# Performance work log

Hardware: AMD Instinct MI355X
Metric: run time of the kernel (lower is better)

The kernel has to match this reference:

```python
import jax, jax.numpy as jnp
import numpy as np

B, S, IN, H = 8, 8192, 64, 256
HEADS, DH, M, L = 8, 32, 64, 4
FF, NC = 4 * H, 2


def setup_inputs() -> dict:
    key = jax.random.key(0)
    ks = jax.random.split(key, 16)
    w = lambda k, shape, s=0.02: jax.random.normal(k, shape, jnp.float32) * s
    return {
        "x": jax.random.normal(ks[0], (B, S, IN), jnp.float32),
        "emb_w": w(ks[1], (IN, H)), "emb_b": jnp.zeros((H,), jnp.float32),
        "pos": jax.random.normal(ks[2], (1, S, H), jnp.float32),
        "ln1_g": jnp.ones((L, H), jnp.float32), "ln1_b": jnp.zeros((L, H), jnp.float32),
        "wq": w(ks[3], (L, H, H)), "wk": w(ks[4], (L, H, H)), "wv": w(ks[5], (L, H, H)),
        "wo": w(ks[6], (L, H, H)), "bo": jnp.zeros((L, H), jnp.float32),
        "ln2_g": jnp.ones((L, H), jnp.float32), "ln2_b": jnp.zeros((L, H), jnp.float32),
        "w1": w(ks[7], (L, H, FF)), "b1": jnp.zeros((L, FF), jnp.float32),
        "w2": w(ks[8], (L, FF, H)), "b2": jnp.zeros((L, H), jnp.float32),
        "proj": jax.random.normal(ks[9], (L, M, DH), jnp.float32),  # FAVOR+ random features (buffer)
        "fc_w": w(ks[10], (H, NC)), "fc_b": jnp.zeros((NC,), jnp.float32),
    }


def layer_norm(x, g, b, eps=1e-5):
    mu = jnp.mean(x, -1, keepdims=True)
    var = jnp.mean(jnp.square(x - mu), -1, keepdims=True)
    return (x - mu) * jax.lax.rsqrt(var + eps) * g + b


def softmax_kernel(x, proj, is_query, eps=1e-4):
    # performer_pytorch FAVOR+ softmax kernel. x: [b,h,n,d], proj: [m,d]
    normalizer = x.shape[-1] ** -0.25
    ratio = proj.shape[0] ** -0.5
    xp = jnp.einsum('bhnd,md->bhnm', x * normalizer, proj)
    diag = jnp.sum(jnp.square(x), -1, keepdims=True) * (0.5 * normalizer * normalizer)
    if is_query:
        mx = jnp.max(xp, axis=-1, keepdims=True)
    else:
        mx = jnp.max(xp, axis=(-1, -2), keepdims=True)
    return ratio * (jnp.exp(xp - diag - mx) + eps)


def performer_attn(x, wq, wk, wv, wo, bo, proj):
    b, s, h = x.shape
    split = lambda t: t.reshape(b, s, HEADS, DH).transpose(0, 2, 1, 3)
    q, k, v = split(x @ wq), split(x @ wk), split(x @ wv)
    qp = softmax_kernel(q, proj, True)   # [b,h,n,m]
    kp = softmax_kernel(k, proj, False)  # [b,h,n,m]
    d_inv = 1.0 / jnp.einsum('bhnm,bhm->bhn', qp, jnp.sum(kp, axis=2))
    context = jnp.einsum('bhnm,bhne->bhme', kp, v)       # [b,h,m,dh]
    out = jnp.einsum('bhnm,bhme->bhne', qp, context) * d_inv[..., None]
    out = out.transpose(0, 2, 1, 3).reshape(b, s, h)
    return out @ wo + bo


def reference(x, emb_w, emb_b, pos, ln1_g, ln1_b, wq, wk, wv, wo, bo,
              ln2_g, ln2_b, w1, b1, w2, b2, proj, fc_w, fc_b):
    h = x @ emb_w + emb_b + pos[:, :x.shape[1], :]
    for l in range(L):
        h = h + performer_attn(layer_norm(h, ln1_g[l], ln1_b[l]),
                               wq[l], wk[l], wv[l], wo[l], bo[l], proj[l])
        hn = layer_norm(h, ln2_g[l], ln2_b[l])
        h = h + (jax.nn.gelu(hn @ w1[l] + b1[l], approximate=False) @ w2[l] + b2[l])
    pooled = jnp.mean(h, axis=1)
    return pooled @ fc_w + fc_b
```

## Files before the change

kernel.cpp:

```cpp
#include <hip/hip_runtime.h>
#include <math.h>

typedef unsigned short u16;
typedef __attribute__((ext_vector_type(8))) short bf16x8;
typedef __attribute__((ext_vector_type(4))) float f32x4;

static constexpr int D_S = 8192;
static constexpr int D_L = 4;
static constexpr int TOK = 65536;
static constexpr float NORMALIZER = 0.4204482076268573f;
static constexpr float RATIO = 0.125f;
static constexpr float KEPS = 1e-4f;

static constexpr size_t OFF_H     = 0;
static constexpr size_t OFF_XNB   = 16777216;
static constexpr size_t OFF_BIG   = 25165824;
static constexpr size_t OFF_V     = 41943040;
static constexpr size_t OFF_WKP   = 46137344;
static constexpr size_t OFF_WQP   = 46268416;
static constexpr size_t OFF_WK    = 46399488;
static constexpr size_t OFF_WQ    = 46465024;
static constexpr size_t OFF_WV    = 46530560;
static constexpr size_t OFF_WO    = 46596096;
static constexpr size_t OFF_W1    = 46661632;
static constexpr size_t OFF_W2    = 46923776;
static constexpr size_t OFF_DG    = 47185920;
static constexpr size_t OFF_KMAX  = 47710208;
static constexpr size_t OFF_PART  = 47710272;
static constexpr size_t OFF_PARTK = 49807424;
static constexpr size_t OFF_CTX   = 49872960;
static constexpr size_t OFF_KSUM  = 50004032;
static constexpr size_t OFF_POOL  = 50008128;
static constexpr size_t NEED_BYTES = 200040704;

static constexpr int BTS = 136;

static __device__ __forceinline__ float bf2f(u16 u) {
  return __uint_as_float(((unsigned int)u) << 16);
}
static __device__ __forceinline__ u16 f2bf(float f) {
  unsigned int u = __float_as_uint(f);
  u = (u + 0x7fffu + ((u >> 16) & 1u)) >> 16;
  return (u16)u;
}
static __device__ __forceinline__ float geluf(float v) {
  return 0.5f * v * (1.f + erff(v * 0.70710678118654752f));
}
static __device__ __forceinline__ float dec_max(unsigned int mk) {
  return __uint_as_float((mk & 0x80000000u) ? (mk & 0x7fffffffu) : ~mk);
}

__global__ void report_kernel(float* out, float v) {
  if (threadIdx.x < 16) out[threadIdx.x] = v;
}

__global__ __launch_bounds__(256) void zero_kernel(float* p, int n) {
  int i = blockIdx.x * 256 + threadIdx.x;
  if (i < n) p[i] = 0.f;
}

__global__ __launch_bounds__(256) void xcvt_kernel(const float* __restrict__ x,
                                                   u16* __restrict__ xb) {
  int i4 = (blockIdx.x * 256 + threadIdx.x) * 4;
  float4 v = *(const float4*)(x + i4);
  u16 o[4] = {f2bf(v.x), f2bf(v.y), f2bf(v.z), f2bf(v.w)};
  *(uint2*)(xb + i4) = *(uint2*)o;
}

__global__ __launch_bounds__(256) void ln_kernel(
    const float* __restrict__ src, u16* __restrict__ dst,
    const float* __restrict__ g, const float* __restrict__ b) {
  int wv = threadIdx.x >> 6, lane = threadIdx.x & 63;
  int t = blockIdx.x * 4 + wv;
  const float4 v = *(const float4*)(src + (size_t)t * 256 + lane * 4);
  float s1 = v.x + v.y + v.z + v.w;
  float s2 = v.x * v.x + v.y * v.y + v.z * v.z + v.w * v.w;
  for (int off = 32; off; off >>= 1) {
    s1 += __shfl_xor(s1, off);
    s2 += __shfl_xor(s2, off);
  }
  float mu = s1 * (1.f / 256.f);
  float var = s2 * (1.f / 256.f) - mu * mu;
  float rs = rsqrtf(var + 1e-5f);
  float4 gg = *(const float4*)(g + lane * 4);
  float4 bb = *(const float4*)(b + lane * 4);
  u16 o0 = f2bf((v.x - mu) * rs * gg.x + bb.x);
  u16 o1 = f2bf((v.y - mu) * rs * gg.y + bb.y);
  u16 o2 = f2bf((v.z - mu) * rs * gg.z + bb.z);
  u16 o3 = f2bf((v.w - mu) * rs * gg.w + bb.w);
  uint2 pk;
  pk.x = (unsigned)o0 | ((unsigned)o1 << 16);
  pk.y = (unsigned)o2 | ((unsigned)o3 << 16);
  *(uint2*)(dst + (size_t)t * 256 + lane * 4) = pk;
}

__global__ __launch_bounds__(256) void wsplit_kernel(
    const float* __restrict__ W, u16* __restrict__ Wt, int K, int N, int nb) {
  int i = blockIdx.x * 256 + threadIdx.x;
  int k = i >> nb, n = i & (N - 1);
  float val = W[i];
  u16 hi = f2bf(val);
  u16 lo = f2bf(val - bf2f(hi));
  Wt[(size_t)n * 2 * K + k] = hi;
  Wt[(size_t)n * 2 * K + K + k] = lo;
}

__global__ __launch_bounds__(256) void wprep_kernel(
    const float* __restrict__ wk, const float* __restrict__ wq,
    const float* __restrict__ wv, const float* __restrict__ wo,
    const float* __restrict__ w1, const float* __restrict__ w2,
    const float* __restrict__ proj,
    u16* __restrict__ WKP, u16* __restrict__ WQP,
    u16* __restrict__ WKt, u16* __restrict__ WQt,
    u16* __restrict__ WVt, u16* __restrict__ WOt,
    u16* __restrict__ W1t, u16* __restrict__ W2t,
    unsigned int* __restrict__ kmaxk) {
  int gi = blockIdx.x * 256 + threadIdx.x;
  if (gi < 64) kmaxk[gi] = 0u;
  if (gi < 262144) {
    int i = gi & 131071;
    const float* w = (gi < 131072) ? wk : wq;
    u16* Wt = (gi < 131072) ? WKP : WQP;
    int k = i & 255, n = i >> 8;
    int head = n >> 6, m = n & 63;
    float s = 0.f;
#pragma unroll
    for (int d = 0; d < 32; ++d) s += w[k * 256 + head * 32 + d] * proj[m * 32 + d];
    Wt[(size_t)n * 256 + k] = f2bf(s * NORMALIZER);
  } else if (gi < 393216) {
    int i = gi - 262144;
    const float* W = (i < 65536) ? wk : wq;
    u16* T = (i < 65536) ? WKt : WQt;
    int j = i & 65535;
    int k = j >> 8, n = j & 255;
    T[(size_t)n * 256 + k] = f2bf(W[j]);
  } else if (gi < 524288) {
    int i = gi - 393216;
    const float* W = (i < 65536) ? wv : wo;
    u16* T = (i < 65536) ? WVt : WOt;
    int j = i & 65535;
    int k = j >> 8, n = j & 255;
    float val = W[j];
    u16 hi = f2bf(val);
    u16 lo = f2bf(val - bf2f(hi));
    T[(size_t)n * 512 + k] = hi;
    T[(size_t)n * 512 + 256 + k] = lo;
  } else if (gi < 786432) {
    int i = gi - 524288;
    int k = i >> 10, n = i & 1023;
    W1t[(size_t)n * 256 + k] = f2bf(w1[i]);
  } else {
    int i = gi - 786432;
    int k = i >> 8, n = i & 255;
    W2t[(size_t)n * 1024 + k] = f2bf(w2[i]);
  }
}

template <int EPI, int ACT, int ACC, int OBF, int KM>
__global__ __launch_bounds__(256) void mfma_gemm(
    const u16* __restrict__ A, const u16* __restrict__ Wt,
    const u16* __restrict__ Wt2,
    const float* __restrict__ bias, const float* __restrict__ posP,
    const u16* __restrict__ diagIn,
    float* __restrict__ outF, u16* __restrict__ outB,
    u16* __restrict__ diagOut, unsigned int* __restrict__ kmaxOut,
    int N, int K) {
  __shared__ __align__(16) u16 Als[4096];
  __shared__ __align__(16) u16 Bls[4096];
  const int K2 = K * KM;
  int tid = threadIdx.x;
  int yb = blockIdx.y;
  int bm = blockIdx.x * 128;
  const u16* Wp = Wt;
  int bn = yb * 128;
  if (EPI == 6 && yb >= 4) { Wp = Wt2; bn = (yb - 4) * 128; }
  int w = tid >> 6, lane = tid & 63;
  int wm = w >> 1, wn = w & 1;
  int lr = lane & 15, lq = lane >> 4;
  f32x4 acc[4][4];
#pragma unroll
  for (int i = 0; i < 4; ++i)
#pragma unroll
    for (int j = 0; j < 4; ++j) acc[i][j] = (f32x4){0.f, 0.f, 0.f, 0.f};
  int r0 = tid >> 2, q0 = tid & 3;
  for (int k0 = 0; k0 < K2; k0 += 32) {
    int kk = k0 + q0 * 8;
    int gka = kk & (K - 1);
    uint4 a0 = *(const uint4*)(A + (size_t)(bm + r0) * K + gka);
    uint4 a1 = *(const uint4*)(A + (size_t)(bm + r0 + 64) * K + gka);
    uint4 b0 = *(const uint4*)(Wp + (size_t)(bn + r0) * K2 + kk);
    uint4 b1 = *(const uint4*)(Wp + (size_t)(bn + r0 + 64) * K2 + kk);
    __syncthreads();
    ((uint4*)Als)[q0 * 128 + r0] = a0;
    ((uint4*)Als)[q0 * 128 + r0 + 64] = a1;
    ((uint4*)Bls)[q0 * 128 + r0] = b0;
    ((uint4*)Bls)[q0 * 128 + r0 + 64] = b1;
    __syncthreads();
    bf16x8 af[4], bfr[4];
#pragma unroll
    for (int mi = 0; mi < 4; ++mi)
      af[mi] = ((const bf16x8*)Als)[lq * 128 + wm * 64 + mi * 16 + lr];
#pragma unroll
    for (int ni = 0; ni < 4; ++ni)
      bfr[ni] = ((const bf16x8*)Bls)[lq * 128 + wn * 64 + ni * 16 + lr];
#pragma unroll
    for (int mi = 0; mi < 4; ++mi)
#pragma unroll
      for (int ni = 0; ni < 4; ++ni)
        acc[mi][ni] = __builtin_amdgcn_mfma_f32_16x16x32_bf16(af[mi], bfr[ni], acc[mi][ni], 0, 0, 0);
  }
  if (EPI == 0) {
#pragma unroll
    for (int ni = 0; ni < 4; ++ni) {
      int col = bn + wn * 64 + ni * 16 + lr;
      float bv = bias ? bias[col] : 0.f;
#pragma unroll
      for (int mi = 0; mi < 4; ++mi)
#pragma unroll
        for (int r = 0; r < 4; ++r) {
          int rowg = bm + wm * 64 + mi * 16 + lq * 4 + r;
          float val = acc[mi][ni][r] + bv;
          if (ACT) val = geluf(val);
          size_t o = (size_t)rowg * N + col;
          if (OBF) outB[o] = f2bf(val);
          else if (ACC) outF[o] += val;
          else outF[o] = val;
        }
    }
  }
  if (EPI == 3) {
    int head = (bn + wn * 64) >> 6;
#pragma unroll
    for (int mi = 0; mi < 4; ++mi) {
      float rm[4] = {-3.4e38f, -3.4e38f, -3.4e38f, -3.4e38f};
#pragma unroll
      for (int ni = 0; ni < 4; ++ni)
#pragma unroll
        for (int r = 0; r < 4; ++r) rm[r] = fmaxf(rm[r], acc[mi][ni][r]);
#pragma unroll
      for (int r = 0; r < 4; ++r) {
        float t = rm[r];
        t = fmaxf(t, __shfl_xor(t, 1)); t = fmaxf(t, __shfl_xor(t, 2));
        t = fmaxf(t, __shfl_xor(t, 4)); t = fmaxf(t, __shfl_xor(t, 8));
        rm[r] = t;
      }
#pragma unroll
      for (int r = 0; r < 4; ++r) {
        int rowg = bm + wm * 64 + mi * 16 + lq * 4 + r;
        float dg = bf2f(diagIn[(size_t)rowg * 16 + 8 + head]);
#pragma unroll
        for (int ni = 0; ni < 4; ++ni) {
          int col = bn + wn * 64 + ni * 16 + lr;
          float v = RATIO * (__expf(acc[mi][ni][r] - dg - rm[r]) + KEPS);
          outB[(size_t)rowg * N + col] = f2bf(v);
        }
      }
    }
  }
  if (EPI == 4) {
#pragma unroll
    for (int ni = 0; ni < 4; ++ni) {
      int col = bn + wn * 64 + ni * 16 + lr;
      float bv = bias[col];
#pragma unroll
      for (int mi = 0; mi < 4; ++mi)
#pragma unroll
        for (int r = 0; r < 4; ++r) {
          int rowg = bm + wm * 64 + mi * 16 + lq * 4 + r;
          outF[(size_t)rowg * 256 + col] =
              acc[mi][ni][r] + bv + posP[(size_t)(rowg & (D_S - 1)) * 256 + col];
        }
    }
  }
  if (EPI == 6) {
    if (yb < 4) {
      float mx = -3.4e38f;
#pragma unroll
      for (int mi = 0; mi < 4; ++mi)
#pragma unroll
        for (int ni = 0; ni < 4; ++ni)
#pragma unroll
          for (int r = 0; r < 4; ++r) {
            float v = acc[mi][ni][r];
            mx = fmaxf(mx, v);
            int rowg = bm + wm * 64 + mi * 16 + lq * 4 + r;
            int col = bn + wn * 64 + ni * 16 + lr;
            outB[(size_t)rowg * N + col] = f2bf(v);
          }
#pragma unroll
      for (int off = 1; off < 64; off <<= 1) mx = fmaxf(mx, __shfl_xor(mx, off));
      if (lane == 0) {
        int b = bm >> 13;
        int head = (bn + wn * 64) >> 6;
        unsigned int u = __float_as_uint(mx);
        unsigned int key = (u & 0x80000000u) ? ~u : (u | 0x80000000u);
        atomicMax(kmaxOut + b * 8 + head, key);
      }
    } else {
      const float c05n2 = 0.5f * NORMALIZER * NORMALIZER;
      int hb = (bn + wn * 64) >> 5;
#pragma unroll
      for (int mi = 0; mi < 4; ++mi) {
        float s0[4] = {0.f, 0.f, 0.f, 0.f}, s1[4] = {0.f, 0.f, 0.f, 0.f};
#pragma unroll
        for (int ni = 0; ni < 4; ++ni)
#pragma unroll
          for (int r = 0; r < 4; ++r) {
            float v = acc[mi][ni][r];
            if (ni < 2) s0[r] += v * v; else s1[r] += v * v;
          }
#pragma unroll
        for (int r = 0; r < 4; ++r) {
          float a = s0[r], b = s1[r];
          a += __shfl_xor(a, 1); a += __shfl_xor(a, 2); a += __shfl_xor(a, 4); a += __shfl_xor(a, 8);
          b += __shfl_xor(b, 1); b += __shfl_xor(b, 2); b += __shfl_xor(b, 4); b += __shfl_xor(b, 8);
          if (lr == 0) {
            int rowg = bm + wm * 64 + mi * 16 + lq * 4 + r;
            diagOut[(size_t)rowg * 16 + hb] = f2bf(c05n2 * a);
            diagOut[(size_t)rowg * 16 + hb + 1] = f2bf(c05n2 * b);
          }
        }
      }
    }
  }
}

__global__ __launch_bounds__(256) void ctxaccum_kernel(
    const u16* __restrict__ xp, const u16* __restrict__ v,
    const u16* __restrict__ dg, const unsigned int* __restrict__ kmaxk,
    float* __restrict__ part, float* __restrict__ partk, int hf) {
  __shared__ float kpS[64 * 64];
  __shared__ float vS[64 * 32];
  int tid = threadIdx.x;
  int bl = blockIdx.x >> 3, head = blockIdx.x & 7, c = blockIdx.y;
  int n0l = bl * 8192 + c * 512;
  int bhg = (hf * 4 + bl) * 8 + head;
  int tg0 = hf * 32768 + n0l;
  float mx = dec_max(kmaxk[bhg]);
  int m = tid & 63, eg = tid >> 6;
  float acc[8] = {};
  float ks = 0.f;
  const u16* kpb = xp + (size_t)tg0 * 512 + head * 64;
  const u16* vb = v + (size_t)n0l * 256 + head * 32;
  for (int tile = 0; tile < 8; ++tile) {
    int nb = tile * 64;
    __syncthreads();
#pragma unroll
    for (int i = 0; i < 2; ++i) {
      int idx8 = tid + i * 256;
      int row = idx8 >> 3, c8 = (idx8 & 7) * 8;
      float dgrow = bf2f(dg[(size_t)(tg0 + nb + row) * 16 + head]);
      u16 tmp[8];
      *(uint4*)tmp = *(const uint4*)(kpb + (size_t)(nb + row) * 512 + c8);
#pragma unroll
      for (int j = 0; j < 8; ++j)
        kpS[row * 64 + c8 + j] = RATIO * (__expf(bf2f(tmp[j]) - dgrow - mx) + KEPS);
    }
    {
      int row = tid >> 2, c8 = (tid & 3) * 8;
      u16 tmp[8];
      *(uint4*)tmp = *(const uint4*)(vb + (size_t)(nb + row) * 256 + c8);
#pragma unroll
      for (int j = 0; j < 8; ++j) vS[row * 32 + c8 + j] = bf2f(tmp[j]);
    }
    __syncthreads();
#pragma unroll 4
    for (int n = 0; n < 64; ++n) {
      float kv = kpS[n * 64 + m];
      if (eg == 0) ks += kv;
      const float* vr = &vS[n * 32 + eg * 8];
#pragma unroll
      for (int j = 0; j < 8; ++j) acc[j] += kv * vr[j];
    }
  }
  float* pp = part + ((size_t)bhg * 16 + c) * 2048 + m * 32 + eg * 8;
#pragma unroll
  for (int j = 0; j < 8; ++j) pp[j] = acc[j];
  if (eg == 0) partk[((size_t)bhg * 16 + c) * 64 + m] = ks;
}

__global__ __launch_bounds__(256) void ctxreduce_kernel(
    const float* __restrict__ part, const float* __restrict__ partk,
    float* __restrict__ ctx, float* __restrict__ ksum) {
  int bh = blockIdx.x, tid = threadIdx.x;
#pragma unroll
  for (int i = 0; i < 8; ++i) {
    int idx = tid + i * 256;
    float s = 0.f;
#pragma unroll
    for (int cc = 0; cc < 16; ++cc)
      s += part[((size_t)bh * 16 + cc) * 2048 + idx];
    ctx[(size_t)bh * 2048 + idx] = s;
  }
  if (tid < 64) {
    float s = 0.f;
#pragma unroll
    for (int cc = 0; cc < 16; ++cc) s += partk[((size_t)bh * 16 + cc) * 64 + tid];
    ksum[bh * 64 + tid] = s;
  }
}

__global__ __launch_bounds__(256) void btprep_kernel(
    const float* __restrict__ ctx, const float* __restrict__ ksum,
    u16* __restrict__ Bt) {
  int bh = blockIdx.x, tid = threadIdx.x;
  for (int idx = tid; idx < 48 * 64; idx += 256) {
    int n = idx >> 6, k = idx & 63;
    float v = 0.f;
    if (n < 32) v = ctx[(size_t)bh * 2048 + k * 32 + n];
    else if (n == 32) v = ksum[bh * 64 + k];
    u16 hi = f2bf(v);
    u16 lo = f2bf(v - bf2f(hi));
    u16* row = Bt + ((size_t)bh * 48 + n) * BTS;
    row[k] = hi;
    row[64 + k] = lo;
  }
}

__global__ __launch_bounds__(256) void attnout_kernel(
    const u16* __restrict__ qp, const u16* __restrict__ Bt,
    u16* __restrict__ ao, int hf) {
  __shared__ __align__(16) u16 BtS[48 * BTS];
  int tid = threadIdx.x;
  int rb = blockIdx.x, head = blockIdx.y;
  int t0l = rb * 128;
  int bhg = ((hf * 32768 + t0l) >> 13) * 8 + head;
  {
    const uint4* src = (const uint4*)(Bt + (size_t)bhg * 48 * BTS);
    for (int i = tid; i < 48 * BTS / 8; i += 256) ((uint4*)BtS)[i] = src[i];
  }
  __syncthreads();
  int w = tid >> 6, lane = tid & 63;
  int lr = lane & 15, lq = lane >> 4;
  int tw = t0l + w * 32;
  const u16* qpb = qp + (size_t)(hf * 32768 + tw) * 512 + head * 64;
  bf16x8 af[2][2];
#pragma unroll
  for (int mt = 0; mt < 2; ++mt)
#pragma unroll
    for (int kc = 0; kc < 2; ++kc)
      af[mt][kc] = *(const bf16x8*)(qpb + (size_t)(mt * 16 + lr) * 512 + kc * 32 + lq * 8);
  f32x4 c0[2], c1[2], c2[2];
#pragma unroll
  for (int mt = 0; mt < 2; ++mt) {
    c0[mt] = (f32x4){0.f, 0.f, 0.f, 0.f};
    c1[mt] = (f32x4){0.f, 0.f, 0.f, 0.f};
    c2[mt] = (f32x4){0.f, 0.f, 0.f, 0.f};
  }
#pragma unroll
  for (int kc = 0; kc < 4; ++kc) {
    bf16x8 b0 = *(const bf16x8*)(BtS + (size_t)(0 * 16 + lr) * BTS + kc * 32 + lq * 8);
    bf16x8 b1 = *(const bf16x8*)(BtS + (size_t)(1 * 16 + lr) * BTS + kc * 32 + lq * 8);
    bf16x8 b2 = *(const bf16x8*)(BtS + (size_t)(2 * 16 + lr) * BTS + kc * 32 + lq * 8);
#pragma unroll
    for (int mt = 0; mt < 2; ++mt) {
      bf16x8 a = af[mt][kc & 1];
      c0[mt] = __builtin_amdgcn_mfma_f32_16x16x32_bf16(a, b0, c0[mt], 0, 0, 0);
      c1[mt] = __builtin_amdgcn_mfma_f32_16x16x32_bf16(a, b1, c1[mt], 0, 0, 0);
      c2[mt] = __builtin_amdgcn_mfma_f32_16x16x32_bf16(a, b2, c2[mt], 0, 0, 0);
    }
  }
#pragma unroll
  for (int mt = 0; mt < 2; ++mt)
#pragma unroll
    for (int r = 0; r < 4; ++r) {
      float den = __shfl(c2[mt][r], lane & 48);
      int rowl = tw + mt * 16 + lq * 4 + r;
      float inv = 1.f / den;
      ao[(size_t)rowl * 256 + head * 32 + lr] = f2bf(c0[mt][r] * inv);
      ao[(size_t)rowl * 256 + head * 32 + 16 + lr] = f2bf(c1[mt][r] * inv);
    }
}

__global__ __launch_bounds__(256) void pool_kernel(
    const float* __restrict__ h, float* __restrict__ pooled) {
  int b = blockIdx.x, chunk = blockIdx.y, j = threadIdx.x;
  const float* hp = h + (size_t)(b * D_S + chunk * 256) * 256 + j;
  float acc = 0.f;
#pragma unroll 4
  for (int s = 0; s < 256; ++s) acc += hp[(size_t)s * 256];
  atomicAdd(pooled + b * 256 + j, acc);
}

__global__ __launch_bounds__(64) void final_kernel(
    const float* __restrict__ pooled, const float* __restrict__ fcw,
    const float* __restrict__ fcb, float* __restrict__ out) {
  int tid = threadIdx.x;
  if (tid >= 16) return;
  int b = tid >> 1, c = tid & 1;
  float acc = 0.f;
  for (int j = 0; j < 256; ++j) acc += pooled[b * 256 + j] * fcw[j * 2 + c];
  out[b * 2 + c] = acc * (1.f / 8192.f) + fcb[c];
}

extern "C" void kernel_launch(void* const* d_in, const int* in_sizes, int n_in,
                              void* d_out, int out_size, void* d_ws, size_t ws_size,
                              hipStream_t stream) {
  const float* x     = (const float*)d_in[0];
  const float* emb_w = (const float*)d_in[1];
  const float* emb_b = (const float*)d_in[2];
  const float* pos   = (const float*)d_in[3];
  const float* ln1_g = (const float*)d_in[4];
  const float* ln1_b = (const float*)d_in[5];
  const float* wq    = (const float*)d_in[6];
  const float* wk    = (const float*)d_in[7];
  const float* wv    = (const float*)d_in[8];
  const float* wo    = (const float*)d_in[9];
  const float* bo    = (const float*)d_in[10];
  const float* ln2_g = (const float*)d_in[11];
  const float* ln2_b = (const float*)d_in[12];
  const float* w1    = (const float*)d_in[13];
  const float* b1    = (const float*)d_in[14];
  const float* w2    = (const float*)d_in[15];
  const float* b2    = (const float*)d_in[16];
  const float* proj  = (const float*)d_in[17];
  const float* fc_w  = (const float*)d_in[18];
  const float* fc_b  = (const float*)d_in[19];

  if (ws_size < NEED_BYTES) {
    report_kernel<<<1, 64, 0, stream>>>((float*)d_out, (float)ws_size);
    return;
  }

  float* ws = (float*)d_ws;
  float* h      = ws + OFF_H;
  u16* xnb      = (u16*)(ws + OFF_XNB);
  u16* BIG      = (u16*)(ws + OFF_BIG);
  u16* Vb       = (u16*)(ws + OFF_V);
  u16* WKPt     = (u16*)(ws + OFF_WKP);
  u16* WQPt     = (u16*)(ws + OFF_WQP);
  u16* WKt      = (u16*)(ws + OFF_WK);
  u16* WQt      = (u16*)(ws + OFF_WQ);
  u16* WVt      = (u16*)(ws + OFF_WV);
  u16* WOt      = (u16*)(ws + OFF_WO);
  u16* W1t      = (u16*)(ws + OFF_W1);
  u16* W2t      = (u16*)(ws + OFF_W2);
  u16* dg       = (u16*)(ws + OFF_DG);
  unsigned int* kmaxk = (unsigned int*)(ws + OFF_KMAX);
  float* part   = ws + OFF_PART;
  u16* Bt       = (u16*)(ws + OFF_PART);
  float* partk  = ws + OFF_PARTK;
  float* ctx    = ws + OFF_CTX;
  float* ksum   = ws + OFF_KSUM;
  float* pooled = ws + OFF_POOL;

  xcvt_kernel<<<4096, 256, 0, stream>>>(x, BIG);
  wsplit_kernel<<<64, 256, 0, stream>>>(emb_w, WKPt, 64, 256, 8);
  mfma_gemm<4, 0, 0, 0, 2><<<dim3(512, 2), 256, 0, stream>>>(
      BIG, WKPt, nullptr, emb_b, pos, nullptr, h, nullptr, nullptr, nullptr, 256, 64);

  for (int l = 0; l < D_L; ++l) {
    const float* pj = proj + l * 2048;
    ln_kernel<<<TOK / 4, 256, 0, stream>>>(h, xnb, ln1_g + l * 256, ln1_b + l * 256);
    wprep_kernel<<<4096, 256, 0, stream>>>(
        wk + l * 65536, wq + l * 65536, wv + l * 65536, wo + l * 65536,
        w1 + l * 262144, w2 + l * 262144, pj,
        WKPt, WQPt, WKt, WQt, WVt, WOt, W1t, W2t, kmaxk);

    mfma_gemm<6, 0, 0, 1, 1><<<dim3(512, 8), 256, 0, stream>>>(
        xnb, WKPt, WKt, nullptr, nullptr, nullptr, nullptr, BIG, dg, kmaxk, 512, 256);
    for (int hf = 0; hf < 2; ++hf) {
      const u16* xh = xnb + (size_t)hf * 32768 * 256;
      mfma_gemm<0, 0, 0, 1, 2><<<dim3(256, 2), 256, 0, stream>>>(
          xh, WVt, nullptr, nullptr, nullptr, nullptr, nullptr, Vb, nullptr, nullptr, 256, 256);
      ctxaccum_kernel<<<dim3(32, 16), 256, 0, stream>>>(BIG, Vb, dg, kmaxk, part, partk, hf);
    }
    ctxreduce_kernel<<<64, 256, 0, stream>>>(part, partk, ctx, ksum);
    btprep_kernel<<<64, 256, 0, stream>>>(ctx, ksum, Bt);
    mfma_gemm<3, 0, 0, 1, 1><<<dim3(512, 4), 256, 0, stream>>>(
        xnb, WQPt, nullptr, nullptr, nullptr, dg, nullptr, BIG, nullptr, nullptr, 512, 256);
    for (int hf = 0; hf < 2; ++hf) {
      float* hh = h + (size_t)hf * 32768 * 256;
      attnout_kernel<<<dim3(256, 8), 256, 0, stream>>>(BIG, Bt, Vb, hf);
      mfma_gemm<0, 0, 1, 0, 2><<<dim3(256, 2), 256, 0, stream>>>(
          Vb, WOt, nullptr, bo + l * 256, nullptr, nullptr, hh, nullptr, nullptr, nullptr, 256, 256);
    }

    ln_kernel<<<TOK / 4, 256, 0, stream>>>(h, xnb, ln2_g + l * 256, ln2_b + l * 256);
    for (int hf = 0; hf < 2; ++hf) {
      const u16* xh = xnb + (size_t)hf * 32768 * 256;
      float* hh = h + (size_t)hf * 32768 * 256;
      mfma_gemm<0, 1, 0, 1, 1><<<dim3(256, 8), 256, 0, stream>>>(
          xh, W1t, nullptr, b1 + l * 1024, nullptr, nullptr, nullptr, BIG, nullptr, nullptr, 1024, 256);
      mfma_gemm<0, 0, 1, 0, 1><<<dim3(256, 2), 256, 0, stream>>>(
          BIG, W2t, nullptr, b2 + l * 256, nullptr, nullptr, hh, nullptr, nullptr, nullptr, 256, 1024);
    }
  }

  zero_kernel<<<8, 256, 0, stream>>>(pooled, 2048);
  pool_kernel<<<dim3(8, 32), 256, 0, stream>>>(h, pooled);
  final_kernel<<<1, 64, 0, stream>>>(pooled, fc_w, fc_b, (float*)d_out);
}
```

Baseline: 2.536 ms.

## Double GEMM K-tile to 64, fuse ctx reduce with Bt prep, drop split embed

The shared MFMA GEMM now stages a 64-wide K slice per iteration, with 4 loads per thread and two MFMA sub-steps. This halves the number of barrier pairs and loop iterations, at the cost of more LDS and registers. The context reduction now writes the hi/lo bf16 Bt layout directly, which removes the btprep kernel and the ctx/ksum round-trip. Bt gets its own buffer. The embedding weight is converted to a single bf16 instead of a hi/lo split, which halves K for the embedding GEMM but lowers its precision.

```diff
diff --git a/kernel.cpp b/kernel.cpp
--- a/kernel.cpp
+++ b/kernel.cpp
@@ -31,7 +31,8 @@
 static constexpr size_t OFF_CTX   = 49872960;
 static constexpr size_t OFF_KSUM  = 50004032;
 static constexpr size_t OFF_POOL  = 50008128;
-static constexpr size_t NEED_BYTES = 200040704;
+static constexpr size_t OFF_BT    = 50010176;
+static constexpr size_t NEED_BYTES = 200876288;
 
 static constexpr int BTS = 136;
 
@@ -94,15 +95,11 @@
   *(uint2*)(dst + (size_t)t * 256 + lane * 4) = pk;
 }
 
-__global__ __launch_bounds__(256) void wsplit_kernel(
-    const float* __restrict__ W, u16* __restrict__ Wt, int K, int N, int nb) {
+__global__ __launch_bounds__(256) void wsplit1_kernel(
+    const float* __restrict__ W, u16* __restrict__ Wt) {
   int i = blockIdx.x * 256 + threadIdx.x;
-  int k = i >> nb, n = i & (N - 1);
-  float val = W[i];
-  u16 hi = f2bf(val);
-  u16 lo = f2bf(val - bf2f(hi));
-  Wt[(size_t)n * 2 * K + k] = hi;
-  Wt[(size_t)n * 2 * K + K + k] = lo;
+  int k = i >> 8, n = i & 255;
+  Wt[(size_t)n * 64 + k] = f2bf(W[i]);
 }
 
 __global__ __launch_bounds__(256) void wprep_kernel(
@@ -165,8 +162,8 @@
     float* __restrict__ outF, u16* __restrict__ outB,
     u16* __restrict__ diagOut, unsigned int* __restrict__ kmaxOut,
     int N, int K) {
-  __shared__ __align__(16) u16 Als[4096];
-  __shared__ __align__(16) u16 Bls[4096];
+  __shared__ __align__(16) u16 Als[8192];
+  __shared__ __align__(16) u16 Bls[8192];
   const int K2 = K * KM;
   int tid = threadIdx.x;
   int yb = blockIdx.y;
@@ -182,44 +179,52 @@
   for (int i = 0; i < 4; ++i)
 #pragma unroll
     for (int j = 0; j < 4; ++j) acc[i][j] = (f32x4){0.f, 0.f, 0.f, 0.f};
-  int r0 = tid >> 2, q0 = tid & 3;
-  for (int k0 = 0; k0 < K2; k0 += 32) {
+  int r0 = tid >> 3, q0 = tid & 7;
+  for (int k0 = 0; k0 < K2; k0 += 64) {
     int kk = k0 + q0 * 8;
     int gka = kk & (K - 1);
-    uint4 a0 = *(const uint4*)(A + (size_t)(bm + r0) * K + gka);
-    uint4 a1 = *(const uint4*)(A + (size_t)(bm + r0 + 64) * K + gka);
-    uint4 b0 = *(const uint4*)(Wp + (size_t)(bn + r0) * K2 + kk);
-    uint4 b1 = *(const uint4*)(Wp + (size_t)(bn + r0 + 64) * K2 + kk);
+    uint4 av[4], bv[4];
+#pragma unroll
+    for (int u = 0; u < 4; ++u) {
+      int row = r0 + u * 32;
+      av[u] = *(const uint4*)(A + (size_t)(bm + row) * K + gka);
+      bv[u] = *(const uint4*)(Wp + (size_t)(bn + row) * K2 + kk);
+    }
     __syncthreads();
-    ((uint4*)Als)[q0 * 128 + r0] = a0;
-    ((uint4*)Als)[q0 * 128 + r0 + 64] = a1;
-    ((uint4*)Bls)[q0 * 128 + r0] = b0;
-    ((uint4*)Bls)[q0 * 128 + r0 + 64] = b1;
+#pragma unroll
+    for (int u = 0; u < 4; ++u) {
+      int row = r0 + u * 32;
+      ((uint4*)Als)[q0 * 128 + row] = av[u];
+      ((uint4*)Bls)[q0 * 128 + row] = bv[u];
+    }
     __syncthreads();
-    bf16x8 af[4], bfr[4];
-#pragma unroll
-    for (int mi = 0; mi < 4; ++mi)
-      af[mi] = ((const bf16x8*)Als)[lq * 128 + wm * 64 + mi * 16 + lr];
-#pragma unroll
-    for (int ni = 0; ni < 4; ++ni)
-      bfr[ni] = ((const bf16x8*)Bls)[lq * 128 + wn * 64 + ni * 16 + lr];
-#pragma unroll
-    for (int mi = 0; mi < 4; ++mi)
+#pragma unroll
+    for (int s = 0; s < 2; ++s) {
+      bf16x8 af[4], bfr[4];
+#pragma unroll
+      for (int mi = 0; mi < 4; ++mi)
+        af[mi] = ((const bf16x8*)Als)[(s * 4 + lq) * 128 + wm * 64 + mi * 16 + lr];
 #pragma unroll
       for (int ni = 0; ni < 4; ++ni)
-        acc[mi][ni] = __builtin_amdgcn_mfma_f32_16x16x32_bf16(af[mi], bfr[ni], acc[mi][ni], 0, 0, 0);
+        bfr[ni] = ((const bf16x8*)Bls)[(s * 4 + lq) * 128 + wn * 64 + ni * 16 + lr];
+#pragma unroll
+      for (int mi = 0; mi < 4; ++mi)
+#pragma unroll
+        for (int ni = 0; ni < 4; ++ni)
+          acc[mi][ni] = __builtin_amdgcn_mfma_f32_16x16x32_bf16(af[mi], bfr[ni], acc[mi][ni], 0, 0, 0);
+    }
   }
   if (EPI == 0) {
 #pragma unroll
     for (int ni = 0; ni < 4; ++ni) {
       int col = bn + wn * 64 + ni * 16 + lr;
-      float bv = bias ? bias[col] : 0.f;
+      float bv2 = bias ? bias[col] : 0.f;
 #pragma unroll
       for (int mi = 0; mi < 4; ++mi)
 #pragma unroll
         for (int r = 0; r < 4; ++r) {
           int rowg = bm + wm * 64 + mi * 16 + lq * 4 + r;
-          float val = acc[mi][ni][r] + bv;
+          float val = acc[mi][ni][r] + bv2;
           if (ACT) val = geluf(val);
           size_t o = (size_t)rowg * N + col;
           if (OBF) outB[o] = f2bf(val);
@@ -261,14 +266,14 @@
 #pragma unroll
     for (int ni = 0; ni < 4; ++ni) {
       int col = bn + wn * 64 + ni * 16 + lr;
-      float bv = bias[col];
+      float bv2 = bias[col];
 #pragma unroll
       for (int mi = 0; mi < 4; ++mi)
 #pragma unroll
         for (int r = 0; r < 4; ++r) {
           int rowg = bm + wm * 64 + mi * 16 + lq * 4 + r;
           outF[(size_t)rowg * 256 + col] =
-              acc[mi][ni][r] + bv + posP[(size_t)(rowg & (D_S - 1)) * 256 + col];
+              acc[mi][ni][r] + bv2 + posP[(size_t)(rowg & (D_S - 1)) * 256 + col];
         }
     }
   }
@@ -381,7 +386,7 @@
 
 __global__ __launch_bounds__(256) void ctxreduce_kernel(
     const float* __restrict__ part, const float* __restrict__ partk,
-    float* __restrict__ ctx, float* __restrict__ ksum) {
+    u16* __restrict__ Bt) {
   int bh = blockIdx.x, tid = threadIdx.x;
 #pragma unroll
   for (int i = 0; i < 8; ++i) {
@@ -390,30 +395,26 @@
 #pragma unroll
     for (int cc = 0; cc < 16; ++cc)
       s += part[((size_t)bh * 16 + cc) * 2048 + idx];
-    ctx[(size_t)bh * 2048 + idx] = s;
+    int e = idx & 31, m = idx >> 5;
+    u16 hi = f2bf(s);
+    u16 lo = f2bf(s - bf2f(hi));
+    u16* row = Bt + ((size_t)bh * 48 + e) * BTS;
+    row[m] = hi;
+    row[64 + m] = lo;
   }
   if (tid < 64) {
     float s = 0.f;
 #pragma unroll
     for (int cc = 0; cc < 16; ++cc) s += partk[((size_t)bh * 16 + cc) * 64 + tid];
-    ksum[bh * 64 + tid] = s;
-  }
-}
-
-__global__ __launch_bounds__(256) void btprep_kernel(
-    const float* __restrict__ ctx, const float* __restrict__ ksum,
-    u16* __restrict__ Bt) {
-  int bh = blockIdx.x, tid = threadIdx.x;
-  for (int idx = tid; idx < 48 * 64; idx += 256) {
-    int n = idx >> 6, k = idx & 63;
-    float v = 0.f;
-    if (n < 32) v = ctx[(size_t)bh * 2048 + k * 32 + n];
-    else if (n == 32) v = ksum[bh * 64 + k];
-    u16 hi = f2bf(v);
-    u16 lo = f2bf(v - bf2f(hi));
-    u16* row = Bt + ((size_t)bh * 48 + n) * BTS;
-    row[k] = hi;
-    row[64 + k] = lo;
+    u16 hi = f2bf(s);
+    u16 lo = f2bf(s - bf2f(hi));
+    u16* row = Bt + ((size_t)bh * 48 + 32) * BTS;
+    row[tid] = hi;
+    row[64 + tid] = lo;
+  }
+  for (int z = tid; z < 15 * 128; z += 256) {
+    int n = 33 + (z >> 7), k = z & 127;
+    Bt[((size_t)bh * 48 + n) * BTS + k] = 0;
   }
 }
 
@@ -538,15 +539,13 @@
   u16* dg       = (u16*)(ws + OFF_DG);
   unsigned int* kmaxk = (unsigned int*)(ws + OFF_KMAX);
   float* part   = ws + OFF_PART;
-  u16* Bt       = (u16*)(ws + OFF_PART);
   float* partk  = ws + OFF_PARTK;
-  float* ctx    = ws + OFF_CTX;
-  float* ksum   = ws + OFF_KSUM;
+  u16* Bt       = (u16*)(ws + OFF_BT);
   float* pooled = ws + OFF_POOL;
 
   xcvt_kernel<<<4096, 256, 0, stream>>>(x, BIG);
-  wsplit_kernel<<<64, 256, 0, stream>>>(emb_w, WKPt, 64, 256, 8);
-  mfma_gemm<4, 0, 0, 0, 2><<<dim3(512, 2), 256, 0, stream>>>(
+  wsplit1_kernel<<<64, 256, 0, stream>>>(emb_w, WKPt);
+  mfma_gemm<4, 0, 0, 0, 1><<<dim3(512, 2), 256, 0, stream>>>(
       BIG, WKPt, nullptr, emb_b, pos, nullptr, h, nullptr, nullptr, nullptr, 256, 64);
 
   for (int l = 0; l < D_L; ++l) {
@@ -565,8 +564,7 @@
           xh, WVt, nullptr, nullptr, nullptr, nullptr, nullptr, Vb, nullptr, nullptr, 256, 256);
       ctxaccum_kernel<<<dim3(32, 16), 256, 0, stream>>>(BIG, Vb, dg, kmaxk, part, partk, hf);
     }
-    ctxreduce_kernel<<<64, 256, 0, stream>>>(part, partk, ctx, ksum);
-    btprep_kernel<<<64, 256, 0, stream>>>(ctx, ksum, Bt);
+    ctxreduce_kernel<<<64, 256, 0, stream>>>(part, partk, Bt);
     mfma_gemm<3, 0, 0, 1, 1><<<dim3(512, 4), 256, 0, stream>>>(
         xnb, WQPt, nullptr, nullptr, nullptr, dg, nullptr, BIG, nullptr, nullptr, 512, 256);
     for (int hf = 0; hf < 2; ++hf) {
```

Measured after the change: 4.277 ms. 1.69x slower.
